# Kernel tuning notes

Measured on AMD Instinct MI355X. Metric: run time of the kernel, lower is better.

Reference implementation:

```python
import jax, jax.numpy as jnp
import numpy as np

NUM_HEADS = 16
HEAD_DIM = 64
HIDDEN = NUM_HEADS * HEAD_DIM
LN_EPS = 1e-6


def setup_inputs() -> dict:
    key = jax.random.key(0)
    ks = jax.random.split(key, 5)
    B, T, H = 2, 2048, HIDDEN
    s = 1.0 / np.sqrt(H)
    return {
        "h": jax.random.normal(ks[0], (B, T, H), jnp.float32),
        "Wq": jax.random.normal(ks[1], (H, H), jnp.float32) * s,
        "bq": jnp.zeros((H,), jnp.float32),
        "Wk": jax.random.normal(ks[2], (H, H), jnp.float32) * s,
        "bk": jnp.zeros((H,), jnp.float32),
        "Wv": jax.random.normal(ks[3], (H, H), jnp.float32) * s,
        "bv": jnp.zeros((H,), jnp.float32),
        "Wo": jax.random.normal(ks[4], (H, H), jnp.float32) * s,
        "bo": jnp.zeros((H,), jnp.float32),
        "gamma": jnp.ones((H,), jnp.float32),
        "beta": jnp.zeros((H,), jnp.float32),
    }


def _split_heads(x):
    B, T, H = x.shape
    return x.reshape(B, T, NUM_HEADS, HEAD_DIM).transpose(0, 2, 1, 3)  # [B,h,T,d]


def reference(h, Wq, bq, Wk, bk, Wv, bv, Wo, bo, gamma, beta):
    # QKV projections (nn.Linear: x @ W^T + b)
    Q = _split_heads(h @ Wq.T + bq)
    K = _split_heads(h @ Wk.T + bk)
    V = _split_heads(h @ Wv.T + bv)
    scale = HEAD_DIM ** -0.5
    scores = jnp.einsum("bhqd,bhkd->bhqk", Q, K) * scale  # [B,h,T,T]
    attn = jax.nn.softmax(scores, axis=-1)
    ctx = jnp.einsum("bhqk,bhkd->bhqd", attn, V)          # [B,h,T,d]
    B, _, T, _ = ctx.shape
    ctx = ctx.transpose(0, 2, 1, 3).reshape(B, T, HIDDEN)
    out = ctx @ Wo.T + bo + h  # dropout is identity at eval
    # LayerNorm(eps=1e-6)
    mu = out.mean(-1, keepdims=True)
    var = jnp.mean((out - mu) ** 2, -1, keepdims=True)
    return (out - mu) * jax.lax.rsqrt(var + LN_EPS) * gamma + beta
```

## Files before the change

### kernel.cpp

```cpp
#include <hip/hip_runtime.h>
#include <hip/hip_bf16.h>

#define NH   16
#define HD   64
#define HID  1024
#define TSEQ 2048
#define BATCH 2
#define KSCALE 0.18033688011112042f

typedef __attribute__((ext_vector_type(4))) float f32x4;
typedef __attribute__((ext_vector_type(8))) short s16x8;
typedef __attribute__((ext_vector_type(4))) short s16x4;
typedef __attribute__((ext_vector_type(8))) _Float16 f16x8;
typedef __attribute__((ext_vector_type(4))) _Float16 f16x4;
typedef __attribute__((ext_vector_type(2))) _Float16 f16x2;

__device__ __forceinline__ unsigned short f2bf(float f) {
  union { float f; unsigned int u; } v; v.f = f;
  unsigned int r = v.u + 0x7fffu + ((v.u >> 16) & 1u);
  return (unsigned short)(r >> 16);
}
__device__ __forceinline__ float bf2f(unsigned short b) {
  union { unsigned int u; float f; } v; v.u = ((unsigned int)b) << 16; return v.f;
}

__global__ __launch_bounds__(256) void cast_all_k(
    const float* __restrict__ h,
    const float* __restrict__ w0, const float* __restrict__ w1,
    const float* __restrict__ w2, const float* __restrict__ w3,
    unsigned short* __restrict__ hb, unsigned short* __restrict__ wbase) {
  int i = blockIdx.x * 256 + threadIdx.x;
  const float* src; unsigned short* dst; int idx; float sc = 1.f;
  if (i < 1048576) { src = h; dst = hb; idx = i; }
  else {
    int idx4 = i - 1048576;
    int w = idx4 >> 18;
    idx = idx4 & 262143;
    src = (w == 0) ? w0 : (w == 1) ? w1 : (w == 2) ? w2 : w3;
    dst = wbase + (size_t)(idx4 - idx) * 4;
    if (w == 1) sc = KSCALE;
  }
  float4 v = ((const float4*)src)[idx];
  ushort4 o;
  o.x = f2bf(v.x * sc); o.y = f2bf(v.y * sc); o.z = f2bf(v.z * sc); o.w = f2bf(v.w * sc);
  ((ushort4*)dst)[idx] = o;
}

__global__ __launch_bounds__(256) void gemm_qkv(
    const unsigned short* __restrict__ hb,
    const unsigned short* __restrict__ wq, const unsigned short* __restrict__ wk,
    const unsigned short* __restrict__ wv,
    const float* __restrict__ bq, const float* __restrict__ bk, const float* __restrict__ bv,
    unsigned short* __restrict__ qo, unsigned short* __restrict__ ko,
    unsigned short* __restrict__ vto) {
  __shared__ unsigned short Ash[64 * 32];
  __shared__ unsigned short Bsh[3][64 * 32];
  const int tid = threadIdx.x, lane = tid & 63, wave = tid >> 6;
  const int l15 = lane & 15, quad = lane >> 4;
  const int wn = wave * 16;
  const int bm = blockIdx.y * 64, bn = blockIdx.x * 64;
  const unsigned short* Ag = hb + (size_t)bm * HID;
  const unsigned short* Bg0 = wq + (size_t)bn * HID;
  const unsigned short* Bg1 = wk + (size_t)bn * HID;
  const unsigned short* Bg2 = wv + (size_t)bn * HID;
  const int idx = tid * 8;
  const int rA = idx >> 5, cA = idx & 31;
  const size_t goff = (size_t)rA * HID + cA;

  f32x4 acc[3][4];
#pragma unroll
  for (int m = 0; m < 3; ++m)
#pragma unroll
    for (int i = 0; i < 4; ++i) acc[m][i] = f32x4{0.f, 0.f, 0.f, 0.f};

  s16x8 pa, pb0, pb1, pb2;
  pa  = *(const s16x8*)(Ag  + goff);
  pb0 = *(const s16x8*)(Bg0 + goff);
  pb1 = *(const s16x8*)(Bg1 + goff);
  pb2 = *(const s16x8*)(Bg2 + goff);

  for (int k0 = 0; k0 < HID; k0 += 32) {
    __syncthreads();
    *(s16x8*)(Ash    + idx) = pa;
    *(s16x8*)(Bsh[0] + idx) = pb0;
    *(s16x8*)(Bsh[1] + idx) = pb1;
    *(s16x8*)(Bsh[2] + idx) = pb2;
    __syncthreads();
    if (k0 + 32 < HID) {
      pa  = *(const s16x8*)(Ag  + goff + k0 + 32);
      pb0 = *(const s16x8*)(Bg0 + goff + k0 + 32);
      pb1 = *(const s16x8*)(Bg1 + goff + k0 + 32);
      pb2 = *(const s16x8*)(Bg2 + goff + k0 + 32);
    }
    s16x8 af[4];
#pragma unroll
    for (int i = 0; i < 4; ++i)
      af[i] = *(const s16x8*)(Ash + (i * 16 + l15) * 32 + quad * 8);
#pragma unroll
    for (int m = 0; m < 3; ++m) {
      s16x8 bfr = *(const s16x8*)(Bsh[m] + (wn + l15) * 32 + quad * 8);
#pragma unroll
      for (int i = 0; i < 4; ++i)
        acc[m][i] = __builtin_amdgcn_mfma_f32_16x16x32_bf16(af[i], bfr, acc[m][i], 0, 0, 0);
    }
  }

  const int col = bn + wn + l15;
  const int head = col >> 6, d = col & 63;
  {
    const float bb = bq[col];
#pragma unroll
    for (int i = 0; i < 4; ++i) {
#pragma unroll
      for (int r = 0; r < 4; ++r) {
        const int row = bm + i * 16 + quad * 4 + r;
        const int bI = row >> 11, t = row & 2047;
        qo[(((size_t)(bI * NH + head) * TSEQ) + t) * HD + d] = f2bf(acc[0][i][r] + bb);
      }
    }
  }
  {
    const float bb = bk[col] * KSCALE;
#pragma unroll
    for (int i = 0; i < 4; ++i) {
#pragma unroll
      for (int r = 0; r < 4; ++r) {
        const int row = bm + i * 16 + quad * 4 + r;
        const int bI = row >> 11, t = row & 2047;
        ko[(((size_t)(bI * NH + head) * TSEQ) + t) * HD + d] = f2bf(acc[1][i][r] + bb);
      }
    }
  }
  {
    const float bb = bv[col];
#pragma unroll
    for (int i = 0; i < 4; ++i) {
      const int row0 = bm + i * 16 + quad * 4;
      const int bI = row0 >> 11, t0 = row0 & 2047;
      unsigned short o[4];
#pragma unroll
      for (int r = 0; r < 4; ++r) {
        _Float16 hv = (_Float16)(acc[2][i][r] + bb);
        o[r] = __builtin_bit_cast(unsigned short, hv);
      }
      *(s16x4*)(vto + ((size_t)((bI * NH + head) * HD + d)) * TSEQ + t0) = *(const s16x4*)o;
    }
  }
}

__global__ __launch_bounds__(256) void gemm_out(
    const unsigned short* __restrict__ ctx, const unsigned short* __restrict__ wo,
    const float* __restrict__ bo, const float* __restrict__ hres,
    float* __restrict__ outf) {
  __shared__ unsigned short Ash[128 * 32];
  __shared__ unsigned short Bsh[64 * 32];
  const int tid = threadIdx.x, lane = tid & 63, wave = tid >> 6;
  const int l15 = lane & 15, quad = lane >> 4;
  const int wm = (wave >> 1) * 64, wn = (wave & 1) * 32;
  const int bm = blockIdx.y * 128, bn = blockIdx.x * 64;
  const unsigned short* Ag = ctx + (size_t)bm * HID;
  const unsigned short* Bg = wo + (size_t)bn * HID;
  const int idx0 = tid * 8, idx1 = idx0 + 2048;
  const int r0 = idx0 >> 5, c0 = idx0 & 31;
  const int r1 = idx1 >> 5, c1 = idx1 & 31;
  const size_t g0 = (size_t)r0 * HID + c0, g1 = (size_t)r1 * HID + c1;
  f32x4 acc[4][2];
#pragma unroll
  for (int i = 0; i < 4; ++i)
#pragma unroll
    for (int j = 0; j < 2; ++j) acc[i][j] = f32x4{0.f, 0.f, 0.f, 0.f};

  s16x8 pa0 = *(const s16x8*)(Ag + g0);
  s16x8 pa1 = *(const s16x8*)(Ag + g1);
  s16x8 pb  = *(const s16x8*)(Bg + g0);

  for (int k0 = 0; k0 < HID; k0 += 32) {
    __syncthreads();
    *(s16x8*)(Ash + idx0) = pa0;
    *(s16x8*)(Ash + idx1) = pa1;
    *(s16x8*)(Bsh + idx0) = pb;
    __syncthreads();
    if (k0 + 32 < HID) {
      pa0 = *(const s16x8*)(Ag + g0 + k0 + 32);
      pa1 = *(const s16x8*)(Ag + g1 + k0 + 32);
      pb  = *(const s16x8*)(Bg + g0 + k0 + 32);
    }
    s16x8 af[4], bfr[2];
#pragma unroll
    for (int i = 0; i < 4; ++i)
      af[i] = *(const s16x8*)(Ash + (wm + i * 16 + l15) * 32 + quad * 8);
#pragma unroll
    for (int j = 0; j < 2; ++j)
      bfr[j] = *(const s16x8*)(Bsh + (wn + j * 16 + l15) * 32 + quad * 8);
#pragma unroll
    for (int i = 0; i < 4; ++i)
#pragma unroll
      for (int j = 0; j < 2; ++j)
        acc[i][j] = __builtin_amdgcn_mfma_f32_16x16x32_bf16(af[i], bfr[j], acc[i][j], 0, 0, 0);
  }
#pragma unroll
  for (int j = 0; j < 2; ++j) {
    const int col = bn + wn + j * 16 + l15;
    const float bb = bo[col];
#pragma unroll
    for (int i = 0; i < 4; ++i) {
#pragma unroll
      for (int r = 0; r < 4; ++r) {
        const int row = bm + wm + i * 16 + quad * 4 + r;
        const size_t off = (size_t)row * HID + col;
        outf[off] = acc[i][j][r] + bb + hres[off];
      }
    }
  }
}

__global__ __launch_bounds__(256, 2) void attn_k(
    const unsigned short* __restrict__ qb, const unsigned short* __restrict__ kb,
    const unsigned short* __restrict__ vt, unsigned short* __restrict__ ctx,
    unsigned short* __restrict__ Opart, float* __restrict__ rsumP,
    int lsplit, int ntiles) {
  __shared__ unsigned short Ksh[64 * 72];
  __shared__ unsigned short Vsh[64 * 72];

  const int tid = threadIdx.x, lane = tid & 63, wave = tid >> 6;
  const int l15 = lane & 15, quad = lane >> 4;
  const int z = blockIdx.z;
  const int b = z >> lsplit;
  const int part = z & ((1 << lsplit) - 1);
  const int h = blockIdx.y, qt = blockIdx.x;
  const size_t ho = ((size_t)(b * NH + h)) * TSEQ * HD;
  const unsigned short* Qh = qb + ho;
  const unsigned short* Kh = kb + ho;
  const unsigned short* Vh = vt + ho;
  const int q0 = qt * 128 + wave * 32;
  const int kt0 = part * ntiles;

  s16x8 qf[2][2];
#pragma unroll
  for (int s = 0; s < 2; ++s)
#pragma unroll
    for (int ks = 0; ks < 2; ++ks)
      qf[s][ks] = *(const s16x8*)(Qh + (size_t)(q0 + s * 16 + l15) * HD + ks * 32 + quad * 8);

  f32x4 accO[4][2];
  float rsum[2];
#pragma unroll
  for (int n2 = 0; n2 < 4; ++n2)
#pragma unroll
    for (int s = 0; s < 2; ++s) accO[n2][s] = f32x4{0.f, 0.f, 0.f, 0.f};
  rsum[0] = rsum[1] = 0.f;

  const int sr = tid >> 3, sc = (tid & 7) * 8;
  s16x8 kreg[2], vreg[2];
#pragma unroll
  for (int hf = 0; hf < 2; ++hf) {
    kreg[hf] = *(const s16x8*)(Kh + (size_t)(kt0 * 64 + sr + hf * 32) * HD + sc);
    vreg[hf] = *(const s16x8*)(Vh + (size_t)(sr + hf * 32) * TSEQ + kt0 * 64 + sc);
  }

  for (int kt = 0; kt < ntiles; ++kt) {
    __syncthreads();
#pragma unroll
    for (int hf = 0; hf < 2; ++hf) {
      *(s16x8*)(Ksh + (sr + hf * 32) * 72 + sc) = kreg[hf];
      *(s16x8*)(Vsh + (sr + hf * 32) * 72 + sc) = vreg[hf];
    }
    __syncthreads();
    if (kt + 1 < ntiles) {
      const int k0n = (kt0 + kt + 1) * 64;
#pragma unroll
      for (int hf = 0; hf < 2; ++hf) {
        kreg[hf] = *(const s16x8*)(Kh + (size_t)(k0n + sr + hf * 32) * HD + sc);
        vreg[hf] = *(const s16x8*)(Vh + (size_t)(sr + hf * 32) * TSEQ + k0n + sc);
      }
    }

    f32x4 accS[2][4];
#pragma unroll
    for (int s = 0; s < 2; ++s)
#pragma unroll
      for (int n = 0; n < 4; ++n) accS[s][n] = f32x4{0.f, 0.f, 0.f, 0.f};
#pragma unroll
    for (int ks = 0; ks < 2; ++ks) {
#pragma unroll
      for (int n = 0; n < 4; ++n) {
        s16x8 kf = *(const s16x8*)(Ksh + (n * 16 + l15) * 72 + ks * 32 + quad * 8);
#pragma unroll
        for (int s = 0; s < 2; ++s)
          accS[s][n] = __builtin_amdgcn_mfma_f32_16x16x32_bf16(kf, qf[s][ks], accS[s][n], 0, 0, 0);
      }
    }

    f16x4 pB[2][4];
#pragma unroll
    for (int s = 0; s < 2; ++s)
#pragma unroll
      for (int n = 0; n < 4; ++n) {
        float e0 = __builtin_amdgcn_exp2f(accS[s][n][0]);
        float e1 = __builtin_amdgcn_exp2f(accS[s][n][1]);
        float e2 = __builtin_amdgcn_exp2f(accS[s][n][2]);
        float e3 = __builtin_amdgcn_exp2f(accS[s][n][3]);
        rsum[s] += (e0 + e1) + (e2 + e3);
        f16x2 lo = __builtin_bit_cast(f16x2, __builtin_amdgcn_cvt_pkrtz(e0, e1));
        f16x2 hi = __builtin_bit_cast(f16x2, __builtin_amdgcn_cvt_pkrtz(e2, e3));
        pB[s][n] = f16x4{lo[0], lo[1], hi[0], hi[1]};
      }

#pragma unroll
    for (int n = 0; n < 4; ++n) {
#pragma unroll
      for (int n2 = 0; n2 < 4; ++n2) {
        f16x4 vA = *(const f16x4*)(Vsh + (n2 * 16 + l15) * 72 + n * 16 + quad * 4);
#pragma unroll
        for (int s = 0; s < 2; ++s)
          accO[n2][s] = __builtin_amdgcn_mfma_f32_16x16x16f16(vA, pB[s][n], accO[n2][s], 0, 0, 0);
      }
    }
  }

#pragma unroll
  for (int s = 0; s < 2; ++s) {
    float t = rsum[s];
    t += __shfl_xor(t, 16, 64);
    t += __shfl_xor(t, 32, 64);
    rsum[s] = t;
  }

  if (lsplit) {
    const int slot = (part * BATCH + b) * NH + h;
    const size_t ob = (size_t)slot * TSEQ * HD;
#pragma unroll
    for (int s = 0; s < 2; ++s) {
      const int t = q0 + s * 16 + l15;
#pragma unroll
      for (int n2 = 0; n2 < 4; ++n2) {
        const int d0 = n2 * 16 + quad * 4;
        unsigned short o[4];
#pragma unroll
        for (int r = 0; r < 4; ++r) o[r] = f2bf(accO[n2][s][r]);
        *(s16x4*)(Opart + ob + (size_t)t * HD + d0) = *(const s16x4*)o;
      }
    }
    if (quad == 0) {
      const size_t rb = (size_t)slot * TSEQ;
#pragma unroll
      for (int s = 0; s < 2; ++s)
        rsumP[rb + q0 + s * 16 + l15] = rsum[s];
    }
  } else {
#pragma unroll
    for (int s = 0; s < 2; ++s) {
      const int t = q0 + s * 16 + l15;
      const float inv = 1.f / rsum[s];
#pragma unroll
      for (int n2 = 0; n2 < 4; ++n2) {
        const int d0 = n2 * 16 + quad * 4;
        unsigned short o[4];
#pragma unroll
        for (int r = 0; r < 4; ++r) o[r] = f2bf(accO[n2][s][r] * inv);
        *(s16x4*)(ctx + ((size_t)(b * TSEQ + t)) * HID + h * HD + d0) = *(const s16x4*)o;
      }
    }
  }
}

__global__ __launch_bounds__(256) void combine_k(
    const unsigned short* __restrict__ Opart, const float* __restrict__ rsumP,
    unsigned short* __restrict__ ctx, int nparts) {
  const int gtid = blockIdx.x * 256 + threadIdx.x;
  const int d = (gtid & 7) * 8;
  const int rem = gtid >> 3;
  const int t = rem & 2047;
  const int bh = rem >> 11;
  float acc[8] = {0, 0, 0, 0, 0, 0, 0, 0};
  float rs = 0.f;
  for (int p = 0; p < nparts; ++p) {
    const int slot = p * 32 + bh;
    s16x8 a = *(const s16x8*)(Opart + ((size_t)slot * TSEQ + t) * HD + d);
#pragma unroll
    for (int j = 0; j < 8; ++j) acc[j] += bf2f(((const unsigned short*)&a)[j]);
    rs += rsumP[(size_t)slot * TSEQ + t];
  }
  const float inv = 1.f / rs;
  unsigned short o[8];
#pragma unroll
  for (int j = 0; j < 8; ++j) o[j] = f2bf(acc[j] * inv);
  const int b = bh >> 4, h = bh & 15;
  *(s16x8*)(ctx + ((size_t)(b * TSEQ + t)) * HID + h * HD + d) = *(const s16x8*)o;
}

__global__ __launch_bounds__(256) void ln_k(float* __restrict__ io,
                                            const float* __restrict__ gamma,
                                            const float* __restrict__ beta) {
  const int row = blockIdx.x, tid = threadIdx.x;
  float x[4]; float s = 0.f, s2 = 0.f;
#pragma unroll
  for (int i = 0; i < 4; ++i) {
    x[i] = io[(size_t)row * HID + tid + i * 256];
    s += x[i]; s2 += x[i] * x[i];
  }
#pragma unroll
  for (int off = 1; off < 64; off <<= 1) {
    s  += __shfl_xor(s, off, 64);
    s2 += __shfl_xor(s2, off, 64);
  }
  __shared__ float red[8];
  const int wave = tid >> 6;
  if ((tid & 63) == 0) { red[wave] = s; red[wave + 4] = s2; }
  __syncthreads();
  s  = red[0] + red[1] + red[2] + red[3];
  s2 = red[4] + red[5] + red[6] + red[7];
  const float mean = s * (1.f / HID);
  const float var  = s2 * (1.f / HID) - mean * mean;
  const float rstd = rsqrtf(var + 1e-6f);
#pragma unroll
  for (int i = 0; i < 4; ++i) {
    const int col = tid + i * 256;
    io[(size_t)row * HID + col] = (x[i] - mean) * rstd * gamma[col] + beta[col];
  }
}

extern "C" void kernel_launch(void* const* d_in, const int* in_sizes, int n_in,
                              void* d_out, int out_size, void* d_ws, size_t ws_size,
                              hipStream_t stream) {
  const float* h    = (const float*)d_in[0];
  const float* Wq   = (const float*)d_in[1];
  const float* bq   = (const float*)d_in[2];
  const float* Wk   = (const float*)d_in[3];
  const float* bk   = (const float*)d_in[4];
  const float* Wv   = (const float*)d_in[5];
  const float* bv   = (const float*)d_in[6];
  const float* Wo   = (const float*)d_in[7];
  const float* bo   = (const float*)d_in[8];
  const float* gamma = (const float*)d_in[9];
  const float* beta  = (const float*)d_in[10];
  float* out = (float*)d_out;

  unsigned short* hb   = (unsigned short*)d_ws;
  unsigned short* wqb  = hb  + 4194304;
  unsigned short* wkb  = wqb + 1048576;
  unsigned short* wvb  = wkb + 1048576;
  unsigned short* wob  = wvb + 1048576;
  unsigned short* qb   = wob + 1048576;
  unsigned short* kb   = qb  + 4194304;
  unsigned short* vtf  = kb  + 4194304;
  unsigned short* Opart = vtf + 4194304;
  unsigned short* ctxb = hb;

  const size_t base = (size_t)(vtf + 4194304 - hb) * 2;
  int lsplit = 0;
  if (ws_size >= base + 2u * 8388608 + 2u * 262144) lsplit = 1;
  const int nparts = 1 << lsplit;
  float* rsumP = (float*)(Opart + (size_t)nparts * 4194304);

  cast_all_k<<<8192, 256, 0, stream>>>(h, Wq, Wk, Wv, Wo, hb, wqb);
  gemm_qkv<<<dim3(16, 64), 256, 0, stream>>>(hb, wqb, wkb, wvb, bq, bk, bv, qb, kb, vtf);
  attn_k<<<dim3(TSEQ / 128, NH, BATCH << lsplit), 256, 0, stream>>>(
      qb, kb, vtf, ctxb, Opart, rsumP, lsplit, 32 >> lsplit);
  if (lsplit)
    combine_k<<<2048, 256, 0, stream>>>(Opart, rsumP, ctxb, nparts);
  gemm_out<<<dim3(16, 32), 256, 0, stream>>>(ctxb, wob, bo, h, out);
  ln_k<<<4096, 256, 0, stream>>>(out, gamma, beta);
}
```

Baseline: 219.2 us.

## Use direct global-to-LDS loads with double buffering and larger QKV GEMM tiles

Both projection GEMMs now fetch tiles with global_load_lds straight into a double-buffered shared-memory ring, replacing the register-staged copies and cutting one barrier per k-step. The QKV GEMM treats Wq/Wk/Wv as one concatenated weight matrix and uses 128x128 tiles on a 24x32 grid. Each block now computes a 4x4 MFMA grid per wave instead of 3x4 with a shared A fragment. The aim is better operand reuse and overlap of loads with MFMA work. The cost is doubled LDS per block and a reliance on the three weight matrices sitting contiguously in the workspace.

```diff
diff --git a/kernel.cpp b/kernel.cpp
--- a/kernel.cpp
+++ b/kernel.cpp
@@ -22,6 +22,12 @@
 }
 __device__ __forceinline__ float bf2f(unsigned short b) {
   union { unsigned int u; float f; } v; v.u = ((unsigned int)b) << 16; return v.f;
+}
+
+__device__ __forceinline__ void gll16(const void* g, void* l) {
+  __builtin_amdgcn_global_load_lds(
+      (const __attribute__((address_space(1))) unsigned int*)g,
+      (__attribute__((address_space(3))) unsigned int*)l, 16, 0, 0);
 }
 
 __global__ __launch_bounds__(256) void cast_all_k(
@@ -48,102 +54,99 @@
 
 __global__ __launch_bounds__(256) void gemm_qkv(
     const unsigned short* __restrict__ hb,
-    const unsigned short* __restrict__ wq, const unsigned short* __restrict__ wk,
-    const unsigned short* __restrict__ wv,
+    const unsigned short* __restrict__ wcat,
     const float* __restrict__ bq, const float* __restrict__ bk, const float* __restrict__ bv,
     unsigned short* __restrict__ qo, unsigned short* __restrict__ ko,
     unsigned short* __restrict__ vto) {
-  __shared__ unsigned short Ash[64 * 32];
-  __shared__ unsigned short Bsh[3][64 * 32];
+  __shared__ unsigned short Ash[2][128 * 32];
+  __shared__ unsigned short Bsh[2][128 * 32];
   const int tid = threadIdx.x, lane = tid & 63, wave = tid >> 6;
   const int l15 = lane & 15, quad = lane >> 4;
-  const int wn = wave * 16;
-  const int bm = blockIdx.y * 64, bn = blockIdx.x * 64;
-  const unsigned short* Ag = hb + (size_t)bm * HID;
-  const unsigned short* Bg0 = wq + (size_t)bn * HID;
-  const unsigned short* Bg1 = wk + (size_t)bn * HID;
-  const unsigned short* Bg2 = wv + (size_t)bn * HID;
-  const int idx = tid * 8;
-  const int rA = idx >> 5, cA = idx & 31;
-  const size_t goff = (size_t)rA * HID + cA;
-
-  f32x4 acc[3][4];
-#pragma unroll
-  for (int m = 0; m < 3; ++m)
-#pragma unroll
-    for (int i = 0; i < 4; ++i) acc[m][i] = f32x4{0.f, 0.f, 0.f, 0.f};
-
-  s16x8 pa, pb0, pb1, pb2;
-  pa  = *(const s16x8*)(Ag  + goff);
-  pb0 = *(const s16x8*)(Bg0 + goff);
-  pb1 = *(const s16x8*)(Bg1 + goff);
-  pb2 = *(const s16x8*)(Bg2 + goff);
+  const int wr = wave >> 1, wc = wave & 1;
+  const int bn = blockIdx.x * 128, bm = blockIdx.y * 128;
+  const char* Ab = (const char*)(hb + (size_t)bm * HID);
+  const char* Bb = (const char*)(wcat + (size_t)bn * HID);
+  const int off = tid * 16;
+  const int r0 = off >> 6, c0 = off & 63;
+  const size_t ga0 = (size_t)r0 * (HID * 2) + c0;
+  const size_t ga1 = (size_t)(r0 + 64) * (HID * 2) + c0;
+  const int lb0 = wave * 512;
+  const int lb1 = 2048 + wave * 512;
+
+  f32x4 acc[4][4];
+#pragma unroll
+  for (int i = 0; i < 4; ++i)
+#pragma unroll
+    for (int j = 0; j < 4; ++j) acc[i][j] = f32x4{0.f, 0.f, 0.f, 0.f};
+
+  gll16(Ab + ga0, &Ash[0][lb0]);
+  gll16(Ab + ga1, &Ash[0][lb1]);
+  gll16(Bb + ga0, &Bsh[0][lb0]);
+  gll16(Bb + ga1, &Bsh[0][lb1]);
+  __syncthreads();
 
   for (int k0 = 0; k0 < HID; k0 += 32) {
+    const int cur = (k0 >> 5) & 1;
+    if (k0 + 32 < HID) {
+      const size_t kb = (size_t)(k0 + 32) * 2;
+      gll16(Ab + ga0 + kb, &Ash[cur ^ 1][lb0]);
+      gll16(Ab + ga1 + kb, &Ash[cur ^ 1][lb1]);
+      gll16(Bb + ga0 + kb, &Bsh[cur ^ 1][lb0]);
+      gll16(Bb + ga1 + kb, &Bsh[cur ^ 1][lb1]);
+    }
+    s16x8 af[4], bfr[4];
+#pragma unroll
+    for (int i = 0; i < 4; ++i)
+      af[i] = *(const s16x8*)(&Ash[cur][(wr * 64 + i * 16 + l15) * 32 + quad * 8]);
+#pragma unroll
+    for (int j = 0; j < 4; ++j)
+      bfr[j] = *(const s16x8*)(&Bsh[cur][(wc * 64 + j * 16 + l15) * 32 + quad * 8]);
+#pragma unroll
+    for (int i = 0; i < 4; ++i)
+#pragma unroll
+      for (int j = 0; j < 4; ++j)
+        acc[i][j] = __builtin_amdgcn_mfma_f32_16x16x32_bf16(af[i], bfr[j], acc[i][j], 0, 0, 0);
     __syncthreads();
-    *(s16x8*)(Ash    + idx) = pa;
-    *(s16x8*)(Bsh[0] + idx) = pb0;
-    *(s16x8*)(Bsh[1] + idx) = pb1;
-    *(s16x8*)(Bsh[2] + idx) = pb2;
-    __syncthreads();
-    if (k0 + 32 < HID) {
-      pa  = *(const s16x8*)(Ag  + goff + k0 + 32);
-      pb0 = *(const s16x8*)(Bg0 + goff + k0 + 32);
-      pb1 = *(const s16x8*)(Bg1 + goff + k0 + 32);
-      pb2 = *(const s16x8*)(Bg2 + goff + k0 + 32);
-    }
-    s16x8 af[4];
-#pragma unroll
-    for (int i = 0; i < 4; ++i)
-      af[i] = *(const s16x8*)(Ash + (i * 16 + l15) * 32 + quad * 8);
-#pragma unroll
-    for (int m = 0; m < 3; ++m) {
-      s16x8 bfr = *(const s16x8*)(Bsh[m] + (wn + l15) * 32 + quad * 8);
-#pragma unroll
-      for (int i = 0; i < 4; ++i)
-        acc[m][i] = __builtin_amdgcn_mfma_f32_16x16x32_bf16(af[i], bfr, acc[m][i], 0, 0, 0);
-    }
-  }
-
-  const int col = bn + wn + l15;
-  const int head = col >> 6, d = col & 63;
-  {
-    const float bb = bq[col];
-#pragma unroll
-    for (int i = 0; i < 4; ++i) {
-#pragma unroll
-      for (int r = 0; r < 4; ++r) {
-        const int row = bm + i * 16 + quad * 4 + r;
-        const int bI = row >> 11, t = row & 2047;
-        qo[(((size_t)(bI * NH + head) * TSEQ) + t) * HD + d] = f2bf(acc[0][i][r] + bb);
-      }
-    }
-  }
-  {
-    const float bb = bk[col] * KSCALE;
-#pragma unroll
-    for (int i = 0; i < 4; ++i) {
-#pragma unroll
-      for (int r = 0; r < 4; ++r) {
-        const int row = bm + i * 16 + quad * 4 + r;
-        const int bI = row >> 11, t = row & 2047;
-        ko[(((size_t)(bI * NH + head) * TSEQ) + t) * HD + d] = f2bf(acc[1][i][r] + bb);
-      }
-    }
-  }
-  {
-    const float bb = bv[col];
-#pragma unroll
-    for (int i = 0; i < 4; ++i) {
-      const int row0 = bm + i * 16 + quad * 4;
-      const int bI = row0 >> 11, t0 = row0 & 2047;
-      unsigned short o[4];
-#pragma unroll
-      for (int r = 0; r < 4; ++r) {
-        _Float16 hv = (_Float16)(acc[2][i][r] + bb);
-        o[r] = __builtin_bit_cast(unsigned short, hv);
-      }
-      *(s16x4*)(vto + ((size_t)((bI * NH + head) * HD + d)) * TSEQ + t0) = *(const s16x4*)o;
+  }
+
+  const int mat = bn >> 10;
+  const int cb = (bn & 1023) + wc * 64;
+  const int rbase = bm + wr * 64;
+  if (mat == 2) {
+#pragma unroll
+    for (int j = 0; j < 4; ++j) {
+      const int coln = cb + j * 16 + l15;
+      const int head = coln >> 6, d = coln & 63;
+      const float bb = bv[coln];
+#pragma unroll
+      for (int i = 0; i < 4; ++i) {
+        const int row0 = rbase + i * 16 + quad * 4;
+        const int bI = row0 >> 11, t0 = row0 & 2047;
+        unsigned short o[4];
+#pragma unroll
+        for (int r = 0; r < 4; ++r) {
+          _Float16 hv = (_Float16)(acc[i][j][r] + bb);
+          o[r] = __builtin_bit_cast(unsigned short, hv);
+        }
+        *(s16x4*)(vto + ((size_t)((bI * NH + head) * HD + d)) * TSEQ + t0) = *(const s16x4*)o;
+      }
+    }
+  } else {
+    unsigned short* dst = (mat == 0) ? qo : ko;
+#pragma unroll
+    for (int j = 0; j < 4; ++j) {
+      const int coln = cb + j * 16 + l15;
+      const int head = coln >> 6, d = coln & 63;
+      const float bb = (mat == 0) ? bq[coln] : bk[coln] * KSCALE;
+#pragma unroll
+      for (int i = 0; i < 4; ++i) {
+#pragma unroll
+        for (int r = 0; r < 4; ++r) {
+          const int row = rbase + i * 16 + quad * 4 + r;
+          const int bI = row >> 11, t = row & 2047;
+          dst[(((size_t)(bI * NH + head) * TSEQ) + t) * HD + d] = f2bf(acc[i][j][r] + bb);
+        }
+      }
     }
   }
 }
@@ -152,63 +155,64 @@
     const unsigned short* __restrict__ ctx, const unsigned short* __restrict__ wo,
     const float* __restrict__ bo, const float* __restrict__ hres,
     float* __restrict__ outf) {
-  __shared__ unsigned short Ash[128 * 32];
-  __shared__ unsigned short Bsh[64 * 32];
+  __shared__ unsigned short Ash[2][128 * 32];
+  __shared__ unsigned short Bsh[2][64 * 32];
   const int tid = threadIdx.x, lane = tid & 63, wave = tid >> 6;
   const int l15 = lane & 15, quad = lane >> 4;
-  const int wm = (wave >> 1) * 64, wn = (wave & 1) * 32;
-  const int bm = blockIdx.y * 128, bn = blockIdx.x * 64;
-  const unsigned short* Ag = ctx + (size_t)bm * HID;
-  const unsigned short* Bg = wo + (size_t)bn * HID;
-  const int idx0 = tid * 8, idx1 = idx0 + 2048;
-  const int r0 = idx0 >> 5, c0 = idx0 & 31;
-  const int r1 = idx1 >> 5, c1 = idx1 & 31;
-  const size_t g0 = (size_t)r0 * HID + c0, g1 = (size_t)r1 * HID + c1;
+  const int wr = wave >> 1, wc = wave & 1;
+  const int bn = blockIdx.x * 64, bm = blockIdx.y * 128;
+  const char* Ab = (const char*)(ctx + (size_t)bm * HID);
+  const char* Bb = (const char*)(wo + (size_t)bn * HID);
+  const int off = tid * 16;
+  const int r0 = off >> 6, c0 = off & 63;
+  const size_t ga0 = (size_t)r0 * (HID * 2) + c0;
+  const size_t ga1 = (size_t)(r0 + 64) * (HID * 2) + c0;
+  const int lb0 = wave * 512, lb1 = 2048 + wave * 512;
+
   f32x4 acc[4][2];
 #pragma unroll
   for (int i = 0; i < 4; ++i)
 #pragma unroll
     for (int j = 0; j < 2; ++j) acc[i][j] = f32x4{0.f, 0.f, 0.f, 0.f};
 
-  s16x8 pa0 = *(const s16x8*)(Ag + g0);
-  s16x8 pa1 = *(const s16x8*)(Ag + g1);
-  s16x8 pb  = *(const s16x8*)(Bg + g0);
+  gll16(Ab + ga0, &Ash[0][lb0]);
+  gll16(Ab + ga1, &Ash[0][lb1]);
+  gll16(Bb + ga0, &Bsh[0][lb0]);
+  __syncthreads();
 
   for (int k0 = 0; k0 < HID; k0 += 32) {
-    __syncthreads();
-    *(s16x8*)(Ash + idx0) = pa0;
-    *(s16x8*)(Ash + idx1) = pa1;
-    *(s16x8*)(Bsh + idx0) = pb;
-    __syncthreads();
+    const int cur = (k0 >> 5) & 1;
     if (k0 + 32 < HID) {
-      pa0 = *(const s16x8*)(Ag + g0 + k0 + 32);
-      pa1 = *(const s16x8*)(Ag + g1 + k0 + 32);
-      pb  = *(const s16x8*)(Bg + g0 + k0 + 32);
+      const size_t kb = (size_t)(k0 + 32) * 2;
+      gll16(Ab + ga0 + kb, &Ash[cur ^ 1][lb0]);
+      gll16(Ab + ga1 + kb, &Ash[cur ^ 1][lb1]);
+      gll16(Bb + ga0 + kb, &Bsh[cur ^ 1][lb0]);
     }
     s16x8 af[4], bfr[2];
 #pragma unroll
     for (int i = 0; i < 4; ++i)
-      af[i] = *(const s16x8*)(Ash + (wm + i * 16 + l15) * 32 + quad * 8);
+      af[i] = *(const s16x8*)(&Ash[cur][(wr * 64 + i * 16 + l15) * 32 + quad * 8]);
 #pragma unroll
     for (int j = 0; j < 2; ++j)
-      bfr[j] = *(const s16x8*)(Bsh + (wn + j * 16 + l15) * 32 + quad * 8);
+      bfr[j] = *(const s16x8*)(&Bsh[cur][(wc * 32 + j * 16 + l15) * 32 + quad * 8]);
 #pragma unroll
     for (int i = 0; i < 4; ++i)
 #pragma unroll
       for (int j = 0; j < 2; ++j)
         acc[i][j] = __builtin_amdgcn_mfma_f32_16x16x32_bf16(af[i], bfr[j], acc[i][j], 0, 0, 0);
+    __syncthreads();
   }
 #pragma unroll
   for (int j = 0; j < 2; ++j) {
-    const int col = bn + wn + j * 16 + l15;
+    const int col = bn + wc * 32 + j * 16 + l15;
     const float bb = bo[col];
 #pragma unroll
     for (int i = 0; i < 4; ++i) {
 #pragma unroll
       for (int r = 0; r < 4; ++r) {
-        const int row = bm + wm + i * 16 + quad * 4 + r;
-        const size_t off = (size_t)row * HID + col;
-        outf[off] = acc[i][j][r] + bb + hres[off];
+        const int row = bm + wr * 64 + i * 16 + quad * 4 + r;
+        const size_t o = (size_t)row * HID + col;
+        outf[o] = acc[i][j][r] + bb + hres[o];
       }
     }
   }
@@ -454,7 +458,7 @@
   float* rsumP = (float*)(Opart + (size_t)nparts * 4194304);
 
   cast_all_k<<<8192, 256, 0, stream>>>(h, Wq, Wk, Wv, Wo, hb, wqb);
-  gemm_qkv<<<dim3(16, 64), 256, 0, stream>>>(hb, wqb, wkb, wvb, bq, bk, bv, qb, kb, vtf);
+  gemm_qkv<<<dim3(24, 32), 256, 0, stream>>>(hb, wqb, bq, bk, bv, qb, kb, vtf);
   attn_k<<<dim3(TSEQ / 128, NH, BATCH << lsplit), 256, 0, stream>>>(
       qb, kb, vtf, ctxb, Opart, rsumP, lsplit, 32 >> lsplit);
   if (lsplit)
```

New measurement: 235.9 us. 1.08x slower.
